# Optimization experiments

Hardware: AMD Instinct MI355X
Metric: run time of the kernel (lower is better)

The kernel has to match this reference:

```python
import jax, jax.numpy as jnp
import numpy as np
from jax import lax

TIME_DIM = 100   # time_feat_dim
MEM_DIM = 172    # node_feat_dim == memory_dim
TAU = 0.3        # energy_threshold
LAM = 0.01       # softshrink sparsity_threshold


def _layer_norm(x, w, b, eps=1e-5):
    m = x.mean(-1, keepdims=True)
    v = ((x - m) ** 2).mean(-1, keepdims=True)
    return (x - m) / jnp.sqrt(v + eps) * w + b


def _time_encode(t):
    # TGN time encoder: cos(t * 1/10^linspace(0,9,D)), fixed (non-trainable)
    freqs = 1.0 / (10.0 ** jnp.linspace(0.0, 9.0, TIME_DIM))
    return jnp.cos(t[..., None] * freqs)


def _softshrink(x, lam=LAM):
    return jnp.where(x > lam, x - lam, jnp.where(x < -lam, x + lam, 0.0))


def setup_inputs() -> dict:
    key = jax.random.key(0)
    ks = jax.random.split(key, 12)
    B, N, NUM_NODES = 8192, 32, 500000
    s = 0.02  # scale used by Global_Local_Filtering
    return {
        "node_ids": jnp.arange(B, dtype=jnp.int32),
        "neighbor_node_ids": jax.random.randint(ks[0], (B, N), 0, NUM_NODES, dtype=jnp.int32),
        "node_interact_times": jax.random.uniform(ks[1], (B,), dtype=jnp.float32) * 1000.0,
        "neighbor_times": jax.random.uniform(ks[2], (B, N), dtype=jnp.float32) * 1000.0,
        "node_memories": jnp.zeros((NUM_NODES, MEM_DIM), jnp.float32),
        "r1": s * jax.random.normal(ks[3], (TIME_DIM, MEM_DIM), jnp.float32),
        "i1": s * jax.random.normal(ks[4], (TIME_DIM, MEM_DIM), jnp.float32),
        "rb1": s * jax.random.normal(ks[5], (MEM_DIM,), jnp.float32),
        "ib1": s * jax.random.normal(ks[6], (MEM_DIM,), jnp.float32),
        "conv_w": 0.02 * jax.random.normal(ks[7], (MEM_DIM, MEM_DIM, 8), jnp.float32),
        "conv_b": 0.02 * jax.random.normal(ks[8], (MEM_DIM,), jnp.float32),
        "rhythm_w": 0.1 * jax.random.normal(ks[9], (272, 1, 4), jnp.float32),
        "lin_w": 0.05 * jax.random.normal(ks[10], (272, MEM_DIM), jnp.float32),
        "lin_b": 0.02 * jax.random.normal(ks[11], (MEM_DIM,), jnp.float32),
        "mb_ln_w": jnp.ones((MEM_DIM,), jnp.float32),
        "mb_ln_b": jnp.zeros((MEM_DIM,), jnp.float32),
        "ln_w": jnp.ones((MEM_DIM,), jnp.float32),
        "ln_b": jnp.zeros((MEM_DIM,), jnp.float32),
    }


def reference(node_ids, neighbor_node_ids, node_interact_times, neighbor_times,
              node_memories, r1, i1, rb1, ib1, conv_w, conv_b,
              rhythm_w, lin_w, lin_b, mb_ln_w, mb_ln_b, ln_w, ln_b):
    # ---- RhythmMemoryUpdater.update_memory ----
    messages = _time_encode(node_interact_times)                 # [B,100]
    old_mem = node_memories[node_ids]                            # [B,172] gather
    x = jnp.concatenate([messages, old_mem], axis=-1)[:, :, None]  # [B,272,1] (NCH)
    # depthwise Conv1d(272,272,k=4,pad=2,groups=272,no bias): length 1 -> 2
    x = lax.conv_general_dilated(x, rhythm_w, (1,), [(2, 2)],
                                 dimension_numbers=("NCH", "OIH", "NCH"),
                                 feature_group_count=272)        # [B,272,2]
    x = jnp.einsum("bcl,cd->bld", x, lin_w) + lin_b              # [B,2,172]
    new_mem = x.mean(axis=1)                                     # mean(dim=1) since 2 != memory_dim
    # set_memories: layer_norm then scatter; then gather + SeqFilter layernorm
    updated = node_memories.at[node_ids].set(_layer_norm(new_mem, mb_ln_w, mb_ln_b))
    gathered = lax.stop_gradient(updated[node_ids])              # memory bank is non-trainable (no_grad)
    root_node_time = _layer_norm(gathered, ln_w, ln_b)           # [B,172]

    # ---- neighbor branch: FSTS (Global_Local_Filtering + Conv1d) ----
    dt = node_interact_times[:, None] - neighbor_times           # [B,N]
    tfeat = _time_encode(dt)                                     # [B,N,100]
    tfeat = jnp.where((neighbor_node_ids == 0)[..., None], 0.0, tfeat)

    xf = jnp.fft.fft(tfeat, axis=1, norm="ortho")                # [B,N,100] complex
    energy = jnp.sum(jnp.abs(xf) ** 2, axis=-1)                  # [B,N]
    mask = (energy / (energy.mean() + 1e-6) >= TAU).astype(tfeat.dtype)
    low = xf * mask[..., None]
    o_r = jnp.einsum("bnc,cd->bnd", low.real, r1) - jnp.einsum("bnc,cd->bnd", low.imag, i1) + rb1
    o_i = jnp.einsum("bnc,cd->bnd", low.imag, r1) + jnp.einsum("bnc,cd->bnd", low.real, i1) + ib1
    y_fft = _softshrink(jax.nn.relu(o_r)) + 1j * _softshrink(jax.nn.relu(o_i))
    y = jnp.fft.ifft(y_fft, axis=1, norm="ortho").real           # [B,N,172]

    # Local_Correlation: Conv1d(172,172,k=8,pad=4) over neighbor axis, then mean over length
    yc = lax.conv_general_dilated(y.transpose(0, 2, 1), conv_w, (1,), [(4, 4)],
                                  dimension_numbers=("NCH", "OIH", "NCH"))
    yc = yc + conv_b[None, :, None]                              # [B,172,33]
    neighbor_out = yc.mean(axis=-1)                              # [B,172]

    return root_node_time + neighbor_out
```

## Files before the change

### kernel.cpp

```cpp
#include <hip/hip_runtime.h>
#include <hip/hip_bf16.h>
#include <math.h>

#define B_ 8192
#define NN 32
#define TD 100
#define MD 172
#define KD 1376
#define TAUC 0.3f
#define LAMC 0.01f

typedef __attribute__((ext_vector_type(8))) short short8;
typedef __attribute__((ext_vector_type(4))) float f32x4;

#define WS_U_OFF    256
#define U_BYTES     ((size_t)B_ * KD * 2)
#define CONVB_ELEMS (11 * 43 * 64 * 8)
#define WBIG_ELEMS  (22 * 7 * 64 * 8)
#define CS_ELEMS    (2 * 64 * 8)
#define ROOT_ELEMS  (11 * 9 * 64 * 8)
#define FRAG_SHORTS (CONVB_ELEMS + WBIG_ELEMS + CS_ELEMS + ROOT_ELEMS)
#define TBL_ELEMS   164

__device__ __forceinline__ float wred(float v) {
#pragma unroll
  for (int o = 32; o > 0; o >>= 1) v += __shfl_down(v, o, 64);
  return v;
}

__device__ __forceinline__ short bf16_bits(float f) {
  __hip_bfloat16 h = __float2bfloat16(f);
  return *(short*)&h;
}

__device__ __forceinline__ unsigned pack2(float a, float b) {
  return (unsigned)(unsigned short)bf16_bits(a) |
         ((unsigned)(unsigned short)bf16_bits(b) << 16);
}

__device__ __forceinline__ float fcos(float x) {
  float r = x * 0.15915494309189535f;
  r = r - floorf(r);
  return __builtin_amdgcn_cosf(r);
}

__global__ __launch_bounds__(256) void k_prep0(
    const float* __restrict__ conv_w, const float* __restrict__ r1,
    const float* __restrict__ i1, const float* __restrict__ rhythm_w,
    const float* __restrict__ lin_w, short* __restrict__ convB,
    short* __restrict__ Wfrag, short* __restrict__ CSfrag,
    short* __restrict__ Rfrag, float* __restrict__ tbl) {
  int idx = blockIdx.x * 256 + threadIdx.x;
  const float inv_s = 0.17677669529663687f;
  if (idx < CONVB_ELEMS) {
    int j = idx & 7;
    int l = (idx >> 3) & 63;
    int s = (idx >> 9) % 43;
    int n0 = idx / (43 * 64 * 8);
    int k = s * 32 + (l >> 4) * 8 + j;
    int col = n0 * 16 + (l & 15);
    float v = (col < MD) ? conv_w[(long)col * KD + k] : 0.f;
    convB[idx] = bf16_bits(v);
    return;
  }
  idx -= CONVB_ELEMS;
  if (idx < WBIG_ELEMS) {
    int j = idx & 7;
    int l = (idx >> 3) & 63;
    int s = (idx % 3584) >> 9;
    int n0 = idx / 3584;
    int k = s * 32 + (l >> 4) * 8 + j;
    int col = n0 * 16 + (l & 15);
    float v = 0.f;
    if (k < 200) {
      if (n0 < 11) {
        int d = col;
        if (d < MD) v = (k < 100) ? r1[k * MD + d] : -i1[(k - 100) * MD + d];
      } else {
        int d = col - 176;
        if (d >= 0 && d < MD) v = (k < 100) ? i1[k * MD + d] : r1[(k - 100) * MD + d];
      }
    }
    Wfrag[idx] = bf16_bits(v);
    return;
  }
  idx -= WBIG_ELEMS;
  if (idx < CS_ELEMS) {
    int j = idx & 7;
    int l = (idx >> 3) & 63;
    int s = idx >> 9;
    int row = l & 15;
    int kq = s * 32 + (l >> 4) * 8 + j;
    float v = 0.f;
    if (row < 8) {
      int kp = (kq < 32) ? kq : kq - 32;
      int lo = row - 4; if (lo < 0) lo = 0;
      int hi = row + 28; if (hi > 31) hi = 31;
      double cs = 0.0, ss = 0.0;
      for (int n = lo; n <= hi; ++n) {
        double ang = 0.19634954084936207740 * (double)((kp * n) & 31);
        cs += cos(ang); ss += sin(ang);
      }
      v = ((kq < 32) ? (float)cs : -(float)ss) * inv_s;
    }
    CSfrag[idx] = bf16_bits(v);
    return;
  }
  idx -= CS_ELEMS;
  if (idx < ROOT_ELEMS) {
    int n = idx / 4608;
    int rem = idx % 4608;
    int s = rem >> 9;
    int l = (rem >> 3) & 63;
    int j = rem & 7;
    int k = s * 32 + (l >> 4) * 8 + j;
    int col = n * 16 + (l & 15);
    float v = 0.f;
    if (k < 272 && col < MD) {
      float hw = 0.5f * (rhythm_w[k * 4 + 1] + rhythm_w[k * 4 + 2]);
      v = hw * lin_w[k * MD + col];
    }
    Rfrag[idx] = bf16_bits(v);
    return;
  }
  idx -= ROOT_ELEMS;
  if (idx < TBL_ELEMS) {
    float v;
    if (idx < 100)      v = (float)exp(-9.0 * (double)idx / 99.0 * 2.302585092994045684);
    else if (idx < 132) v = (float)cos(0.19634954084936207740 * (double)(idx - 100));
    else                v = (float)sin(0.19634954084936207740 * (double)(idx - 132));
    tbl[idx] = v;
  }
}

__global__ __launch_bounds__(256) void k_mean(const int* __restrict__ nid,
                                              const float* __restrict__ t,
                                              const float* __restrict__ nt,
                                              const float* __restrict__ tbl,
                                              float* __restrict__ ws) {
  __shared__ float fr[TD];
  __shared__ float part[4];
  int tid = threadIdx.x;
  if (tid < TD) fr[tid] = tbl[tid];
  __syncthreads();
  int idx = blockIdx.x * 256 + tid;
  int b = idx >> 5;
  float s = 0.f;
  if (nid[idx] != 0) {
    float dt = t[b] - nt[idx];
    for (int c = 0; c < TD; ++c) { float v = fcos(dt * fr[c]); s = fmaf(v, v, s); }
  }
  s = wred(s);
  if ((tid & 63) == 0) part[tid >> 6] = s;
  __syncthreads();
  if (tid == 0) atomicAdd(ws, part[0] + part[1] + part[2] + part[3]);
}

__global__ __launch_bounds__(384, 8) void k_main(
    const int* __restrict__ nbr_id, const float* __restrict__ t,
    const float* __restrict__ nt, const float* __restrict__ rb1,
    const float* __restrict__ ib1, const float* __restrict__ ws0,
    const short* __restrict__ Wfrag, const short* __restrict__ CSfrag,
    const float* __restrict__ tbl, short* __restrict__ u_out) {
  __shared__ __align__(16) short sA[32 * 232];
  __shared__ __align__(16) unsigned char s_un[12800];
  __shared__ float s_fr[TD];
  __shared__ float s_c32[32], s_s32[32], s_dt[32], s_z[32];
  __shared__ float s_energy[32];

  float* tf = (float*)s_un;
  short* Y = (short*)s_un;
  const int tid = threadIdx.x;
  const int b = blockIdx.x;
  const int l = tid & 63, w = tid >> 6;
  const float inv_s = 0.17677669529663687f;

  if (tid < 32) {
    s_c32[tid] = tbl[100 + tid];
    s_s32[tid] = tbl[132 + tid];
    int gi = b * NN + tid;
    int id = nbr_id[gi];
    float d = t[b] - nt[gi];
    s_z[tid]  = (id == 0) ? 0.f : 1.f;
    s_dt[tid] = (id == 0) ? 0.f : d;
    s_energy[tid] = 0.f;
  }
  if (tid < TD) s_fr[tid] = tbl[tid];
  __syncthreads();

  for (int idx = tid; idx < NN * TD; idx += 384) {
    int n = idx / TD, c = idx - n * TD;
    tf[idx] = s_z[n] * fcos(s_dt[n] * s_fr[c]);
  }
  if (tid < 256) {
    int row = tid >> 3, q = tid & 7;
    *(uint2*)(sA + row * 232 + 200 + q * 4) = make_uint2(0u, 0u);
  }
  __syncthreads();

  for (int task = tid; task < 17 * 25; task += 384) {
    int k = task / 25, c4 = (task - k * 25) * 4;
    float ar0=0,ar1=0,ar2=0,ar3=0, ai0=0,ai1=0,ai2=0,ai3=0;
    for (int n = 0; n < NN; ++n) {
      float4 a = *(const float4*)(tf + n * TD + c4);
      int j = (k * n) & 31;
      float cw = s_c32[j], sw = s_s32[j];
      ar0 = fmaf(a.x, cw, ar0); ai0 = fmaf(a.x, -sw, ai0);
      ar1 = fmaf(a.y, cw, ar1); ai1 = fmaf(a.y, -sw, ai1);
      ar2 = fmaf(a.z, cw, ar2); ai2 = fmaf(a.z, -sw, ai2);
      ar3 = fmaf(a.w, cw, ar3); ai3 = fmaf(a.w, -sw, ai3);
    }
    ar0*=inv_s; ar1*=inv_s; ar2*=inv_s; ar3*=inv_s;
    ai0*=inv_s; ai1*=inv_s; ai2*=inv_s; ai3*=inv_s;
    float e = ar0*ar0+ar1*ar1+ar2*ar2+ar3*ar3 + ai0*ai0+ai1*ai1+ai2*ai2+ai3*ai3;
    atomicAdd(&s_energy[k], e);
    uint2 vr = make_uint2(pack2(ar0, ar1), pack2(ar2, ar3));
    uint2 vi = make_uint2(pack2(ai0, ai1), pack2(ai2, ai3));
    *(uint2*)(sA + k * 232 + c4) = vr;
    *(uint2*)(sA + k * 232 + 100 + c4) = vi;
    if (k >= 1 && k <= 15) {
      uint2 vin = make_uint2(pack2(-ai0, -ai1), pack2(-ai2, -ai3));
      *(uint2*)(sA + (32 - k) * 232 + c4) = vr;
      *(uint2*)(sA + (32 - k) * 232 + 100 + c4) = vin;
    }
  }
  __syncthreads();

  {
    float gth = TAUC * (ws0[0] * (1.0f / 262144.0f) + 1e-6f);
    for (int idx = tid; idx < 800; idx += 384) {
      int row = idx / 25, q = idx - row * 25;
      int ks = (row <= 16) ? row : 32 - row;
      if (s_energy[ks] < gth)
        *(uint4*)((char*)sA + row * 464 + q * 16) = make_uint4(0u,0u,0u,0u);
    }
  }
  __syncthreads();

  const int mside = (w >= 3) ? 1 : 0;
  const int wn = w % 3;
  short8 afrag[7];
  {
    const short* ab = sA + (mside * 16 + (l & 15)) * 232 + ((l >> 4) << 3);
#pragma unroll
    for (int s = 0; s < 7; ++s) afrag[s] = *(const short8*)(ab + s * 32);
  }
  for (int n = wn; n < 11; n += 3) {
    f32x4 acc = (f32x4)(0.f);
#pragma unroll
    for (int s = 0; s < 7; ++s) {
      short8 bb = *(const short8*)(Wfrag + (((n * 7 + s) * 64) + l) * 8);
      acc = __builtin_amdgcn_mfma_f32_16x16x32_bf16(afrag[s], bb, acc, 0, 0, 0);
    }
    int d = n * 16 + (l & 15);
    bool valid = (d < MD);
    float bias = valid ? rb1[d] : 0.f;
    float y0 = valid ? fmaxf(acc[0] + bias - LAMC, 0.f) : 0.f;
    float y1 = valid ? fmaxf(acc[1] + bias - LAMC, 0.f) : 0.f;
    float y2 = valid ? fmaxf(acc[2] + bias - LAMC, 0.f) : 0.f;
    float y3 = valid ? fmaxf(acc[3] + bias - LAMC, 0.f) : 0.f;
    *(uint2*)(Y + d * 32 + mside * 16 + ((l >> 4) << 2)) =
        make_uint2(pack2(y0, y1), pack2(y2, y3));
  }
  __syncthreads();

  f32x4 uacc[2];
  uacc[0] = (f32x4)(0.f); uacc[1] = (f32x4)(0.f);
  {
    short8 cs0 = *(const short8*)(CSfrag + (l << 3));
#pragma unroll
    for (int ti = 0; ti < 2; ++ti) {
      int nu = w + 6 * ti;
      if (nu < 11) {
        short8 bfr = *(const short8*)(Y + (nu * 16 + (l & 15)) * 32 + ((l >> 4) << 3));
        uacc[ti] = __builtin_amdgcn_mfma_f32_16x16x32_bf16(cs0, bfr, uacc[ti], 0, 0, 0);
      }
    }
  }
  __syncthreads();

  for (int n = wn; n < 11; n += 3) {
    f32x4 acc = (f32x4)(0.f);
    int nw = n + 11;
#pragma unroll
    for (int s = 0; s < 7; ++s) {
      short8 bb = *(const short8*)(Wfrag + (((nw * 7 + s) * 64) + l) * 8);
      acc = __builtin_amdgcn_mfma_f32_16x16x32_bf16(afrag[s], bb, acc, 0, 0, 0);
    }
    int d = n * 16 + (l & 15);
    bool valid = (d < MD);
    float bias = valid ? ib1[d] : 0.f;
    float y0 = valid ? fmaxf(acc[0] + bias - LAMC, 0.f) : 0.f;
    float y1 = valid ? fmaxf(acc[1] + bias - LAMC, 0.f) : 0.f;
    float y2 = valid ? fmaxf(acc[2] + bias - LAMC, 0.f) : 0.f;
    float y3 = valid ? fmaxf(acc[3] + bias - LAMC, 0.f) : 0.f;
    *(uint2*)(Y + d * 32 + mside * 16 + ((l >> 4) << 2)) =
        make_uint2(pack2(y0, y1), pack2(y2, y3));
  }
  __syncthreads();

  {
    short8 cs1 = *(const short8*)(CSfrag + ((64 + l) << 3));
#pragma unroll
    for (int ti = 0; ti < 2; ++ti) {
      int nu = w + 6 * ti;
      if (nu < 11) {
        short8 bfr = *(const short8*)(Y + (nu * 16 + (l & 15)) * 32 + ((l >> 4) << 3));
        uacc[ti] = __builtin_amdgcn_mfma_f32_16x16x32_bf16(cs1, bfr, uacc[ti], 0, 0, 0);
        int q = l >> 4;
        int d = nu * 16 + (l & 15);
        if (q < 2 && d < MD) {
          uint2 pv = make_uint2(pack2(uacc[ti][0], uacc[ti][1]),
                                pack2(uacc[ti][2], uacc[ti][3]));
          *(uint2*)(u_out + (long)b * KD + d * 8 + q * 4) = pv;
        }
      }
    }
  }
}

__global__ __launch_bounds__(512) void k_tail(
    const int* __restrict__ node_ids, const float* __restrict__ t,
    const float* __restrict__ node_mem, const short* __restrict__ u,
    const short* __restrict__ convB, const float* __restrict__ conv_b,
    const short* __restrict__ Rfrag, const float* __restrict__ lin_b,
    const float* __restrict__ mb_w, const float* __restrict__ mb_b,
    const float* __restrict__ ln_w, const float* __restrict__ ln_b,
    const float* __restrict__ tbl, float* __restrict__ out) {
  __shared__ __align__(16) short aR[16 * 296];
  __shared__ __align__(16) float Ct[16 * 176];
  const int tid = threadIdx.x;
  const int l = tid & 63, w = tid >> 6;
  const int b0 = blockIdx.x * 16;

  for (int idx = tid; idx < 16 * 296; idx += 512) {
    int r = idx / 296, c = idx - r * 296;
    float v = 0.f;
    if (c < TD) v = fcos(t[b0 + r] * tbl[c]);
    else if (c < 272) v = node_mem[(long)node_ids[b0 + r] * MD + (c - TD)];
    aR[idx] = bf16_bits(v);
  }
  __syncthreads();

  const int cstart = (w < 5) ? w * 2 : 10;
  const int ccnt = (w < 5) ? 2 : ((w == 5) ? 1 : 0);
  f32x4 cacc[2];
  cacc[0] = (f32x4)(0.f); cacc[1] = (f32x4)(0.f);
  if (ccnt) {
    const short* ap = u + (long)(b0 + (l & 15)) * KD + ((l >> 4) << 3);
    for (int s = 0; s < 43; ++s) {
      short8 a = *(const short8*)(ap + s * 32);
#pragma unroll
      for (int tt = 0; tt < 2; ++tt) {
        if (tt < ccnt) {
          long n0 = cstart + tt;
          short8 bb = *(const short8*)(convB + ((n0 * 43 + s) * 64 + l) * 8);
          cacc[tt] = __builtin_amdgcn_mfma_f32_16x16x32_bf16(a, bb, cacc[tt], 0, 0, 0);
        }
      }
    }
  }

  const int rstart = (w == 5) ? 0 : ((w == 6) ? 3 : 7);
  const int rcnt = (w == 5) ? 3 : ((w >= 6) ? 4 : 0);
  if (rcnt) {
    f32x4 racc[4];
#pragma unroll
    for (int tt = 0; tt < 4; ++tt) racc[tt] = (f32x4)(0.f);
    const short* arp = aR + (l & 15) * 296 + ((l >> 4) << 3);
    for (int s = 0; s < 9; ++s) {
      short8 a = *(const short8*)(arp + s * 32);
#pragma unroll
      for (int tt = 0; tt < 4; ++tt) {
        if (tt < rcnt) {
          int n = rstart + tt;
          short8 bb = *(const short8*)(Rfrag + (((n * 9 + s) * 64) + l) * 8);
          racc[tt] = __builtin_amdgcn_mfma_f32_16x16x32_bf16(a, bb, racc[tt], 0, 0, 0);
        }
      }
    }
#pragma unroll
    for (int tt = 0; tt < 4; ++tt) {
      if (tt < rcnt) {
        int n = (rstart + tt) * 16 + (l & 15);
        if (n < MD) {
#pragma unroll
          for (int r = 0; r < 4; ++r)
            Ct[((l >> 4) * 4 + r) * 176 + n] = racc[tt][r];
        }
      }
    }
  }
  __syncthreads();

  if (tid < 256) {
    int r = tid >> 4, g = tid & 15;
    float v[11];
    float sm = 0.f, sq = 0.f;
#pragma unroll
    for (int j = 0; j < 11; ++j) {
      int c = g + 16 * j;
      float x = (c < MD) ? (Ct[r * 176 + c] + lin_b[c]) : 0.f;
      v[j] = x; sm += x; sq += x * x;
    }
#pragma unroll
    for (int m = 1; m < 16; m <<= 1) { sm += __shfl_xor(sm, m, 64); sq += __shfl_xor(sq, m, 64); }
    float mean = sm / 172.f;
    float rstd = rsqrtf(sq / 172.f - mean * mean + 1e-5f);
    float sm2 = 0.f, sq2 = 0.f;
#pragma unroll
    for (int j = 0; j < 11; ++j) {
      int c = g + 16 * j;
      if (c < MD) {
        float h = (v[j] - mean) * rstd * mb_w[c] + mb_b[c];
        v[j] = h; sm2 += h; sq2 += h * h;
      }
    }
#pragma unroll
    for (int m = 1; m < 16; m <<= 1) { sm2 += __shfl_xor(sm2, m, 64); sq2 += __shfl_xor(sq2, m, 64); }
    float mean2 = sm2 / 172.f;
    float rstd2 = rsqrtf(sq2 / 172.f - mean2 * mean2 + 1e-5f);
#pragma unroll
    for (int j = 0; j < 11; ++j) {
      int c = g + 16 * j;
      if (c < MD) Ct[r * 176 + c] = (v[j] - mean2) * rstd2 * ln_w[c] + ln_b[c];
    }
  }
  __syncthreads();

#pragma unroll
  for (int tt = 0; tt < 2; ++tt) {
    if (tt < ccnt) {
      int n = (cstart + tt) * 16 + (l & 15);
      if (n < MD) {
        float cb = conv_b[n];
#pragma unroll
        for (int r = 0; r < 4; ++r) {
          int mr = (l >> 4) * 4 + r;
          out[(long)(b0 + mr) * MD + n] =
              Ct[mr * 176 + n] + cacc[tt][r] * (1.0f / 33.0f) + cb;
        }
      }
    }
  }
}

extern "C" void kernel_launch(void* const* d_in, const int* in_sizes, int n_in,
                              void* d_out, int out_size, void* d_ws, size_t ws_size,
                              hipStream_t stream) {
  const int* node_ids = (const int*)d_in[0];
  const int* nbr_id   = (const int*)d_in[1];
  const float* t  = (const float*)d_in[2];
  const float* nt = (const float*)d_in[3];
  const float* node_mem = (const float*)d_in[4];
  const float* r1 = (const float*)d_in[5];
  const float* i1 = (const float*)d_in[6];
  const float* rb1 = (const float*)d_in[7];
  const float* ib1 = (const float*)d_in[8];
  const float* conv_w = (const float*)d_in[9];
  const float* conv_b = (const float*)d_in[10];
  const float* rhythm_w = (const float*)d_in[11];
  const float* lin_w = (const float*)d_in[12];
  const float* lin_b = (const float*)d_in[13];
  const float* mb_w = (const float*)d_in[14];
  const float* mb_b = (const float*)d_in[15];
  const float* ln_w = (const float*)d_in[16];
  const float* ln_b = (const float*)d_in[17];
  float* out = (float*)d_out;
  float* wsf = (float*)d_ws;

  char* base = (char*)d_ws;
  short* u      = (short*)(base + WS_U_OFF);
  short* convB  = (short*)(base + WS_U_OFF + U_BYTES);
  short* Wfrag  = convB + CONVB_ELEMS;
  short* CSfrag = Wfrag + WBIG_ELEMS;
  short* Rfrag  = CSfrag + CS_ELEMS;
  float* tbl    = (float*)(Rfrag + ROOT_ELEMS);

  hipMemsetAsync(d_ws, 0, 16, stream);
  k_prep0<<<(FRAG_SHORTS + TBL_ELEMS + 255) / 256, 256, 0, stream>>>(
      conv_w, r1, i1, rhythm_w, lin_w, convB, Wfrag, CSfrag, Rfrag, tbl);
  k_mean<<<1024, 256, 0, stream>>>(nbr_id, t, nt, tbl, wsf);
  k_main<<<B_, 384, 0, stream>>>(nbr_id, t, nt, rb1, ib1, wsf, Wfrag, CSfrag, tbl, u);
  k_tail<<<512, 512, 0, stream>>>(node_ids, t, node_mem, u, convB, conv_b,
                                  Rfrag, lin_b, mb_w, mb_b, ln_w, ln_b, tbl, out);
}
```

Measured before the change: 615.4 us.

## Split main kernel into DFT and filter kernels, drop separate energy-mean pass

Removes the k_mean kernel by having the new DFT kernel compute per-frequency energies and atomically accumulate the global energy sum. The DFT kernel writes the spectrum straight to global memory in MFMA fragment layout, and a separate filter kernel then applies the energy mask and runs the complex GEMM and inverse DFT. Each wave in the filter kernel handles one batch row with register-resident A fragments, and shares B loads across the real and imaginary outputs. The cost is a large global intermediate (about 117 MB of bf16) that is written and then read back, in exchange for dropping the redundant cosine recomputation in k_mean and improving MFMA occupancy.

```diff
diff --git a/kernel.cpp b/kernel.cpp
--- a/kernel.cpp
+++ b/kernel.cpp
@@ -21,6 +21,7 @@
 #define ROOT_ELEMS  (11 * 9 * 64 * 8)
 #define FRAG_SHORTS (CONVB_ELEMS + WBIG_ELEMS + CS_ELEMS + ROOT_ELEMS)
 #define TBL_ELEMS   164
+#define AFRAG_SHORTS_PER_B 7168
 
 __device__ __forceinline__ float wred(float v) {
 #pragma unroll
@@ -133,47 +134,23 @@
   }
 }
 
-__global__ __launch_bounds__(256) void k_mean(const int* __restrict__ nid,
-                                              const float* __restrict__ t,
-                                              const float* __restrict__ nt,
-                                              const float* __restrict__ tbl,
-                                              float* __restrict__ ws) {
-  __shared__ float fr[TD];
-  __shared__ float part[4];
-  int tid = threadIdx.x;
-  if (tid < TD) fr[tid] = tbl[tid];
-  __syncthreads();
-  int idx = blockIdx.x * 256 + tid;
-  int b = idx >> 5;
-  float s = 0.f;
-  if (nid[idx] != 0) {
-    float dt = t[b] - nt[idx];
-    for (int c = 0; c < TD; ++c) { float v = fcos(dt * fr[c]); s = fmaf(v, v, s); }
-  }
-  s = wred(s);
-  if ((tid & 63) == 0) part[tid >> 6] = s;
-  __syncthreads();
-  if (tid == 0) atomicAdd(ws, part[0] + part[1] + part[2] + part[3]);
-}
-
-__global__ __launch_bounds__(384, 8) void k_main(
+__device__ __forceinline__ void stA(short* __restrict__ ab, int k, int col, uint2 v) {
+  int mside = k >> 4, row = k & 15, s = col >> 5, q = (col >> 3) & 3, j = col & 7;
+  *(uint2*)(ab + (((mside * 7 + s) << 9) + (q << 7) + (row << 3) + j)) = v;
+}
+
+__global__ __launch_bounds__(256) void k_dft(
     const int* __restrict__ nbr_id, const float* __restrict__ t,
-    const float* __restrict__ nt, const float* __restrict__ rb1,
-    const float* __restrict__ ib1, const float* __restrict__ ws0,
-    const short* __restrict__ Wfrag, const short* __restrict__ CSfrag,
-    const float* __restrict__ tbl, short* __restrict__ u_out) {
-  __shared__ __align__(16) short sA[32 * 232];
-  __shared__ __align__(16) unsigned char s_un[12800];
+    const float* __restrict__ nt, const float* __restrict__ tbl,
+    short* __restrict__ Afrag, float* __restrict__ e_arr,
+    float* __restrict__ ws_total) {
+  __shared__ __align__(16) float tf[NN * TD];
   __shared__ float s_fr[TD];
-  __shared__ float s_c32[32], s_s32[32], s_dt[32], s_z[32];
-  __shared__ float s_energy[32];
-
-  float* tf = (float*)s_un;
-  short* Y = (short*)s_un;
+  __shared__ float s_c32[32], s_s32[32], s_dt[32], s_z[32], s_energy[32];
   const int tid = threadIdx.x;
   const int b = blockIdx.x;
-  const int l = tid & 63, w = tid >> 6;
   const float inv_s = 0.17677669529663687f;
+  short* ab = Afrag + (long)b * AFRAG_SHORTS_PER_B;
 
   if (tid < 32) {
     s_c32[tid] = tbl[100 + tid];
@@ -188,17 +165,18 @@
   if (tid < TD) s_fr[tid] = tbl[tid];
   __syncthreads();
 
-  for (int idx = tid; idx < NN * TD; idx += 384) {
+  for (int idx = tid; idx < NN * TD; idx += 256) {
     int n = idx / TD, c = idx - n * TD;
     tf[idx] = s_z[n] * fcos(s_dt[n] * s_fr[c]);
   }
-  if (tid < 256) {
-    int row = tid >> 3, q = tid & 7;
-    *(uint2*)(sA + row * 232 + 200 + q * 4) = make_uint2(0u, 0u);
-  }
-  __syncthreads();
-
-  for (int task = tid; task < 17 * 25; task += 384) {
+  if (tid < 96) {
+    int mside = tid / 48, q = 1 + (tid / 16) % 3, row = tid & 15;
+    *(uint4*)(ab + ((mside * 7 + 6) << 9) + (q << 7) + (row << 3)) =
+        make_uint4(0u, 0u, 0u, 0u);
+  }
+  __syncthreads();
+
+  for (int task = tid; task < 17 * 25; task += 256) {
     int k = task / 25, c4 = (task - k * 25) * 4;
     float ar0=0,ar1=0,ar2=0,ar3=0, ai0=0,ai1=0,ai2=0,ai3=0;
     for (int n = 0; n < NN; ++n) {
@@ -216,105 +194,96 @@
     atomicAdd(&s_energy[k], e);
     uint2 vr = make_uint2(pack2(ar0, ar1), pack2(ar2, ar3));
     uint2 vi = make_uint2(pack2(ai0, ai1), pack2(ai2, ai3));
-    *(uint2*)(sA + k * 232 + c4) = vr;
-    *(uint2*)(sA + k * 232 + 100 + c4) = vi;
+    stA(ab, k, c4, vr);
+    stA(ab, k, 100 + c4, vi);
     if (k >= 1 && k <= 15) {
       uint2 vin = make_uint2(pack2(-ai0, -ai1), pack2(-ai2, -ai3));
-      *(uint2*)(sA + (32 - k) * 232 + c4) = vr;
-      *(uint2*)(sA + (32 - k) * 232 + 100 + c4) = vin;
-    }
-  }
-  __syncthreads();
-
-  {
-    float gth = TAUC * (ws0[0] * (1.0f / 262144.0f) + 1e-6f);
-    for (int idx = tid; idx < 800; idx += 384) {
-      int row = idx / 25, q = idx - row * 25;
-      int ks = (row <= 16) ? row : 32 - row;
-      if (s_energy[ks] < gth)
-        *(uint4*)((char*)sA + row * 464 + q * 16) = make_uint4(0u,0u,0u,0u);
-    }
-  }
-  __syncthreads();
-
-  const int mside = (w >= 3) ? 1 : 0;
-  const int wn = w % 3;
-  short8 afrag[7];
-  {
-    const short* ab = sA + (mside * 16 + (l & 15)) * 232 + ((l >> 4) << 3);
-#pragma unroll
-    for (int s = 0; s < 7; ++s) afrag[s] = *(const short8*)(ab + s * 32);
-  }
-  for (int n = wn; n < 11; n += 3) {
-    f32x4 acc = (f32x4)(0.f);
+      stA(ab, 32 - k, c4, vr);
+      stA(ab, 32 - k, 100 + c4, vin);
+    }
+  }
+  __syncthreads();
+
+  if (tid < 64) {
+    float e = 0.f;
+    if (tid < 32) {
+      int ks = (tid <= 16) ? tid : 32 - tid;
+      e = s_energy[ks];
+      e_arr[b * 32 + tid] = e;
+    }
+    float s = wred(e);
+    if (tid == 0) atomicAdd(ws_total, s);
+  }
+}
+
+__global__ __launch_bounds__(256, 3) void k_filt(
+    const short* __restrict__ Afrag, const short* __restrict__ Wfrag,
+    const short* __restrict__ CSfrag, const float* __restrict__ e_arr,
+    const float* __restrict__ ws0, const float* __restrict__ rb1,
+    const float* __restrict__ ib1, short* __restrict__ u_out) {
+  __shared__ __align__(16) short scr[4][16 * 72];
+  const int tid = threadIdx.x, l = tid & 63, w = tid >> 6;
+  const long b = (long)blockIdx.x * 4 + w;
+  short* S = scr[w];
+  const int c = l & 15, q = l >> 4;
+
+  const float gth = TAUC * (ws0[0] * (1.0f / 262144.0f) + 1e-6f);
+  short8 cs0 = *(const short8*)(CSfrag + l * 8);
+  short8 cs1 = *(const short8*)(CSfrag + (64 + l) * 8);
+
+  const float e0 = e_arr[b * 32 + c];
+  const float e1 = e_arr[b * 32 + 16 + c];
+  const bool m0 = (e0 >= gth), m1 = (e1 >= gth);
+  const short* ab = Afrag + b * AFRAG_SHORTS_PER_B + l * 8;
+  short8 A0[7], A1[7];
+#pragma unroll
+  for (int s = 0; s < 7; ++s) {
+    short8 a = *(const short8*)(ab + (s << 9));
+    short8 bsh = *(const short8*)(ab + 3584 + (s << 9));
+    A0[s] = m0 ? a : (short8)0;
+    A1[s] = m1 ? bsh : (short8)0;
+  }
+
+#pragma unroll 1
+  for (int n = 0; n < 11; ++n) {
+    f32x4 a00 = (f32x4)(0.f), a10 = (f32x4)(0.f);
+    f32x4 a01 = (f32x4)(0.f), a11 = (f32x4)(0.f);
 #pragma unroll
     for (int s = 0; s < 7; ++s) {
-      short8 bb = *(const short8*)(Wfrag + (((n * 7 + s) * 64) + l) * 8);
-      acc = __builtin_amdgcn_mfma_f32_16x16x32_bf16(afrag[s], bb, acc, 0, 0, 0);
-    }
-    int d = n * 16 + (l & 15);
-    bool valid = (d < MD);
-    float bias = valid ? rb1[d] : 0.f;
-    float y0 = valid ? fmaxf(acc[0] + bias - LAMC, 0.f) : 0.f;
-    float y1 = valid ? fmaxf(acc[1] + bias - LAMC, 0.f) : 0.f;
-    float y2 = valid ? fmaxf(acc[2] + bias - LAMC, 0.f) : 0.f;
-    float y3 = valid ? fmaxf(acc[3] + bias - LAMC, 0.f) : 0.f;
-    *(uint2*)(Y + d * 32 + mside * 16 + ((l >> 4) << 2)) =
-        make_uint2(pack2(y0, y1), pack2(y2, y3));
-  }
-  __syncthreads();
-
-  f32x4 uacc[2];
-  uacc[0] = (f32x4)(0.f); uacc[1] = (f32x4)(0.f);
-  {
-    short8 cs0 = *(const short8*)(CSfrag + (l << 3));
-#pragma unroll
-    for (int ti = 0; ti < 2; ++ti) {
-      int nu = w + 6 * ti;
-      if (nu < 11) {
-        short8 bfr = *(const short8*)(Y + (nu * 16 + (l & 15)) * 32 + ((l >> 4) << 3));
-        uacc[ti] = __builtin_amdgcn_mfma_f32_16x16x32_bf16(cs0, bfr, uacc[ti], 0, 0, 0);
-      }
-    }
-  }
-  __syncthreads();
-
-  for (int n = wn; n < 11; n += 3) {
-    f32x4 acc = (f32x4)(0.f);
-    int nw = n + 11;
-#pragma unroll
-    for (int s = 0; s < 7; ++s) {
-      short8 bb = *(const short8*)(Wfrag + (((nw * 7 + s) * 64) + l) * 8);
-      acc = __builtin_amdgcn_mfma_f32_16x16x32_bf16(afrag[s], bb, acc, 0, 0, 0);
-    }
-    int d = n * 16 + (l & 15);
-    bool valid = (d < MD);
-    float bias = valid ? ib1[d] : 0.f;
-    float y0 = valid ? fmaxf(acc[0] + bias - LAMC, 0.f) : 0.f;
-    float y1 = valid ? fmaxf(acc[1] + bias - LAMC, 0.f) : 0.f;
-    float y2 = valid ? fmaxf(acc[2] + bias - LAMC, 0.f) : 0.f;
-    float y3 = valid ? fmaxf(acc[3] + bias - LAMC, 0.f) : 0.f;
-    *(uint2*)(Y + d * 32 + mside * 16 + ((l >> 4) << 2)) =
-        make_uint2(pack2(y0, y1), pack2(y2, y3));
-  }
-  __syncthreads();
-
-  {
-    short8 cs1 = *(const short8*)(CSfrag + ((64 + l) << 3));
-#pragma unroll
-    for (int ti = 0; ti < 2; ++ti) {
-      int nu = w + 6 * ti;
-      if (nu < 11) {
-        short8 bfr = *(const short8*)(Y + (nu * 16 + (l & 15)) * 32 + ((l >> 4) << 3));
-        uacc[ti] = __builtin_amdgcn_mfma_f32_16x16x32_bf16(cs1, bfr, uacc[ti], 0, 0, 0);
-        int q = l >> 4;
-        int d = nu * 16 + (l & 15);
-        if (q < 2 && d < MD) {
-          uint2 pv = make_uint2(pack2(uacc[ti][0], uacc[ti][1]),
-                                pack2(uacc[ti][2], uacc[ti][3]));
-          *(uint2*)(u_out + (long)b * KD + d * 8 + q * 4) = pv;
-        }
-      }
+      short8 b0 = *(const short8*)(Wfrag + (((n * 7 + s) << 6) + l) * 8);
+      short8 b1 = *(const short8*)(Wfrag + ((((n + 11) * 7 + s) << 6) + l) * 8);
+      a00 = __builtin_amdgcn_mfma_f32_16x16x32_bf16(A0[s], b0, a00, 0, 0, 0);
+      a10 = __builtin_amdgcn_mfma_f32_16x16x32_bf16(A1[s], b0, a10, 0, 0, 0);
+      a01 = __builtin_amdgcn_mfma_f32_16x16x32_bf16(A0[s], b1, a01, 0, 0, 0);
+      a11 = __builtin_amdgcn_mfma_f32_16x16x32_bf16(A1[s], b1, a11, 0, 0, 0);
+    }
+    const int d = n * 16 + c;
+    const bool valid = (d < MD);
+    const float br = valid ? rb1[d] : 0.f;
+    const float bi = valid ? ib1[d] : 0.f;
+    f32x4 y00, y10, y01, y11;
+#pragma unroll
+    for (int r = 0; r < 4; ++r) {
+      y00[r] = valid ? fmaxf(a00[r] + br - LAMC, 0.f) : 0.f;
+      y10[r] = valid ? fmaxf(a10[r] + br - LAMC, 0.f) : 0.f;
+      y01[r] = valid ? fmaxf(a01[r] + bi - LAMC, 0.f) : 0.f;
+      y11[r] = valid ? fmaxf(a11[r] + bi - LAMC, 0.f) : 0.f;
+    }
+    asm volatile("s_waitcnt lgkmcnt(0)" ::: "memory");
+    short* Sc = S + c * 72 + q * 4;
+    *(uint2*)(Sc)      = make_uint2(pack2(y00[0], y00[1]), pack2(y00[2], y00[3]));
+    *(uint2*)(Sc + 16) = make_uint2(pack2(y10[0], y10[1]), pack2(y10[2], y10[3]));
+    *(uint2*)(Sc + 32) = make_uint2(pack2(y01[0], y01[1]), pack2(y01[2], y01[3]));
+    *(uint2*)(Sc + 48) = make_uint2(pack2(y11[0], y11[1]), pack2(y11[2], y11[3]));
+    asm volatile("s_waitcnt lgkmcnt(0)" ::: "memory");
+    short8 Br = *(const short8*)(S + c * 72 + q * 8);
+    short8 Bi = *(const short8*)(S + c * 72 + 32 + q * 8);
+    f32x4 u = (f32x4)(0.f);
+    u = __builtin_amdgcn_mfma_f32_16x16x32_bf16(cs0, Br, u, 0, 0, 0);
+    u = __builtin_amdgcn_mfma_f32_16x16x32_bf16(cs1, Bi, u, 0, 0, 0);
+    if (q < 2 && valid) {
+      uint2 pv = make_uint2(pack2(u[0], u[1]), pack2(u[2], u[3]));
+      *(uint2*)(u_out + b * KD + d * 8 + q * 4) = pv;
     }
   }
 }
@@ -476,12 +445,17 @@
   short* CSfrag = Wfrag + WBIG_ELEMS;
   short* Rfrag  = CSfrag + CS_ELEMS;
   float* tbl    = (float*)(Rfrag + ROOT_ELEMS);
+  size_t off = (size_t)((char*)(tbl + TBL_ELEMS) - base);
+  off = (off + 255) & ~(size_t)255;
+  short* Afrag = (short*)(base + off);
+  float* e_arr = (float*)(base + off + (size_t)B_ * AFRAG_SHORTS_PER_B * 2);
 
   hipMemsetAsync(d_ws, 0, 16, stream);
   k_prep0<<<(FRAG_SHORTS + TBL_ELEMS + 255) / 256, 256, 0, stream>>>(
       conv_w, r1, i1, rhythm_w, lin_w, convB, Wfrag, CSfrag, Rfrag, tbl);
-  k_mean<<<1024, 256, 0, stream>>>(nbr_id, t, nt, tbl, wsf);
-  k_main<<<B_, 384, 0, stream>>>(nbr_id, t, nt, rb1, ib1, wsf, Wfrag, CSfrag, tbl, u);
+  k_dft<<<B_, 256, 0, stream>>>(nbr_id, t, nt, tbl, Afrag, e_arr, wsf);
+  k_filt<<<B_ / 4, 256, 0, stream>>>(Afrag, Wfrag, CSfrag, e_arr, wsf,
+                                     rb1, ib1, u);
   k_tail<<<512, 512, 0, stream>>>(node_ids, t, node_mem, u, convB, conv_b,
                                   Rfrag, lin_b, mb_w, mb_b, ln_w, ln_b, tbl, out);
 }
```

Measured after the change: 636.4 us. 1.03x slower.

## Rebalance MFMA work across waves in main and tail kernels

Applied to the files above, without the earlier changes.

In k_main, each wave now loads both 16-row halves of the spectral A-matrix and computes two output column tiles, so each Wfrag B-fragment load is reused for two MFMAs. Previously the six waves were split by row half and column stride. The occupancy hint drops from 8 to 4 blocks to leave room for the larger register set. In k_tail the block grows to 1024 threads: 11 waves each take one conv output tile and 5 waves share the root projection tiles, which evens out per-wave MFMA chains. Lower occupancy in k_main may reduce latency hiding for its global loads.

```diff
diff --git a/kernel.cpp b/kernel.cpp
--- a/kernel.cpp
+++ b/kernel.cpp
@@ -156,7 +156,7 @@
   if (tid == 0) atomicAdd(ws, part[0] + part[1] + part[2] + part[3]);
 }
 
-__global__ __launch_bounds__(384, 8) void k_main(
+__global__ __launch_bounds__(384, 4) void k_main(
     const int* __restrict__ nbr_id, const float* __restrict__ t,
     const float* __restrict__ nt, const float* __restrict__ rb1,
     const float* __restrict__ ib1, const float* __restrict__ ws0,
@@ -173,6 +173,7 @@
   const int tid = threadIdx.x;
   const int b = blockIdx.x;
   const int l = tid & 63, w = tid >> 6;
+  const int c = l & 15, q = l >> 4;
   const float inv_s = 0.17677669529663687f;
 
   if (tid < 32) {
@@ -189,12 +190,12 @@
   __syncthreads();
 
   for (int idx = tid; idx < NN * TD; idx += 384) {
-    int n = idx / TD, c = idx - n * TD;
-    tf[idx] = s_z[n] * fcos(s_dt[n] * s_fr[c]);
+    int n = idx / TD, cc = idx - n * TD;
+    tf[idx] = s_z[n] * fcos(s_dt[n] * s_fr[cc]);
   }
   if (tid < 256) {
-    int row = tid >> 3, q = tid & 7;
-    *(uint2*)(sA + row * 232 + 200 + q * 4) = make_uint2(0u, 0u);
+    int row = tid >> 3, qq = tid & 7;
+    *(uint2*)(sA + row * 232 + 200 + qq * 4) = make_uint2(0u, 0u);
   }
   __syncthreads();
 
@@ -229,38 +230,48 @@
   {
     float gth = TAUC * (ws0[0] * (1.0f / 262144.0f) + 1e-6f);
     for (int idx = tid; idx < 800; idx += 384) {
-      int row = idx / 25, q = idx - row * 25;
+      int row = idx / 25, qq = idx - row * 25;
       int ks = (row <= 16) ? row : 32 - row;
       if (s_energy[ks] < gth)
-        *(uint4*)((char*)sA + row * 464 + q * 16) = make_uint4(0u,0u,0u,0u);
-    }
-  }
-  __syncthreads();
-
-  const int mside = (w >= 3) ? 1 : 0;
-  const int wn = w % 3;
-  short8 afrag[7];
+        *(uint4*)((char*)sA + row * 464 + qq * 16) = make_uint4(0u,0u,0u,0u);
+    }
+  }
+  __syncthreads();
+
+  short8 A0[7], A1[7];
   {
-    const short* ab = sA + (mside * 16 + (l & 15)) * 232 + ((l >> 4) << 3);
-#pragma unroll
-    for (int s = 0; s < 7; ++s) afrag[s] = *(const short8*)(ab + s * 32);
-  }
-  for (int n = wn; n < 11; n += 3) {
-    f32x4 acc = (f32x4)(0.f);
+    const short* a0 = sA + c * 232 + (q << 3);
+    const short* a1 = sA + (16 + c) * 232 + (q << 3);
 #pragma unroll
     for (int s = 0; s < 7; ++s) {
-      short8 bb = *(const short8*)(Wfrag + (((n * 7 + s) * 64) + l) * 8);
-      acc = __builtin_amdgcn_mfma_f32_16x16x32_bf16(afrag[s], bb, acc, 0, 0, 0);
-    }
-    int d = n * 16 + (l & 15);
-    bool valid = (d < MD);
-    float bias = valid ? rb1[d] : 0.f;
-    float y0 = valid ? fmaxf(acc[0] + bias - LAMC, 0.f) : 0.f;
-    float y1 = valid ? fmaxf(acc[1] + bias - LAMC, 0.f) : 0.f;
-    float y2 = valid ? fmaxf(acc[2] + bias - LAMC, 0.f) : 0.f;
-    float y3 = valid ? fmaxf(acc[3] + bias - LAMC, 0.f) : 0.f;
-    *(uint2*)(Y + d * 32 + mside * 16 + ((l >> 4) << 2)) =
-        make_uint2(pack2(y0, y1), pack2(y2, y3));
+      A0[s] = *(const short8*)(a0 + s * 32);
+      A1[s] = *(const short8*)(a1 + s * 32);
+    }
+  }
+
+#pragma unroll
+  for (int rep = 0; rep < 2; ++rep) {
+    int n = w + 6 * rep;
+    if (n < 11) {
+      f32x4 acc0 = (f32x4)(0.f), acc1 = (f32x4)(0.f);
+#pragma unroll
+      for (int s = 0; s < 7; ++s) {
+        short8 bb = *(const short8*)(Wfrag + (((n * 7 + s) << 6) + l) * 8);
+        acc0 = __builtin_amdgcn_mfma_f32_16x16x32_bf16(A0[s], bb, acc0, 0, 0, 0);
+        acc1 = __builtin_amdgcn_mfma_f32_16x16x32_bf16(A1[s], bb, acc1, 0, 0, 0);
+      }
+      int d = n * 16 + c;
+      bool valid = (d < MD);
+      float bias = valid ? rb1[d] : 0.f;
+      f32x4 y0, y1;
+#pragma unroll
+      for (int r = 0; r < 4; ++r) {
+        y0[r] = valid ? fmaxf(acc0[r] + bias - LAMC, 0.f) : 0.f;
+        y1[r] = valid ? fmaxf(acc1[r] + bias - LAMC, 0.f) : 0.f;
+      }
+      *(uint2*)(Y + d * 32 + (q << 2))      = make_uint2(pack2(y0[0], y0[1]), pack2(y0[2], y0[3]));
+      *(uint2*)(Y + d * 32 + 16 + (q << 2)) = make_uint2(pack2(y1[0], y1[1]), pack2(y1[2], y1[3]));
+    }
   }
   __syncthreads();
 
@@ -272,30 +283,37 @@
     for (int ti = 0; ti < 2; ++ti) {
       int nu = w + 6 * ti;
       if (nu < 11) {
-        short8 bfr = *(const short8*)(Y + (nu * 16 + (l & 15)) * 32 + ((l >> 4) << 3));
+        short8 bfr = *(const short8*)(Y + (nu * 16 + c) * 32 + (q << 3));
         uacc[ti] = __builtin_amdgcn_mfma_f32_16x16x32_bf16(cs0, bfr, uacc[ti], 0, 0, 0);
       }
     }
   }
   __syncthreads();
 
-  for (int n = wn; n < 11; n += 3) {
-    f32x4 acc = (f32x4)(0.f);
-    int nw = n + 11;
-#pragma unroll
-    for (int s = 0; s < 7; ++s) {
-      short8 bb = *(const short8*)(Wfrag + (((nw * 7 + s) * 64) + l) * 8);
-      acc = __builtin_amdgcn_mfma_f32_16x16x32_bf16(afrag[s], bb, acc, 0, 0, 0);
-    }
-    int d = n * 16 + (l & 15);
-    bool valid = (d < MD);
-    float bias = valid ? ib1[d] : 0.f;
-    float y0 = valid ? fmaxf(acc[0] + bias - LAMC, 0.f) : 0.f;
-    float y1 = valid ? fmaxf(acc[1] + bias - LAMC, 0.f) : 0.f;
-    float y2 = valid ? fmaxf(acc[2] + bias - LAMC, 0.f) : 0.f;
-    float y3 = valid ? fmaxf(acc[3] + bias - LAMC, 0.f) : 0.f;
-    *(uint2*)(Y + d * 32 + mside * 16 + ((l >> 4) << 2)) =
-        make_uint2(pack2(y0, y1), pack2(y2, y3));
+#pragma unroll
+  for (int rep = 0; rep < 2; ++rep) {
+    int n = w + 6 * rep;
+    if (n < 11) {
+      int nw = n + 11;
+      f32x4 acc0 = (f32x4)(0.f), acc1 = (f32x4)(0.f);
+#pragma unroll
+      for (int s = 0; s < 7; ++s) {
+        short8 bb = *(const short8*)(Wfrag + (((nw * 7 + s) << 6) + l) * 8);
+        acc0 = __builtin_amdgcn_mfma_f32_16x16x32_bf16(A0[s], bb, acc0, 0, 0, 0);
+        acc1 = __builtin_amdgcn_mfma_f32_16x16x32_bf16(A1[s], bb, acc1, 0, 0, 0);
+      }
+      int d = n * 16 + c;
+      bool valid = (d < MD);
+      float bias = valid ? ib1[d] : 0.f;
+      f32x4 y0, y1;
+#pragma unroll
+      for (int r = 0; r < 4; ++r) {
+        y0[r] = valid ? fmaxf(acc0[r] + bias - LAMC, 0.f) : 0.f;
+        y1[r] = valid ? fmaxf(acc1[r] + bias - LAMC, 0.f) : 0.f;
+      }
+      *(uint2*)(Y + d * 32 + (q << 2))      = make_uint2(pack2(y0[0], y0[1]), pack2(y0[2], y0[3]));
+      *(uint2*)(Y + d * 32 + 16 + (q << 2)) = make_uint2(pack2(y1[0], y1[1]), pack2(y1[2], y1[3]));
+    }
   }
   __syncthreads();
 
@@ -305,10 +323,9 @@
     for (int ti = 0; ti < 2; ++ti) {
       int nu = w + 6 * ti;
       if (nu < 11) {
-        short8 bfr = *(const short8*)(Y + (nu * 16 + (l & 15)) * 32 + ((l >> 4) << 3));
+        short8 bfr = *(const short8*)(Y + (nu * 16 + c) * 32 + (q << 3));
         uacc[ti] = __builtin_amdgcn_mfma_f32_16x16x32_bf16(cs1, bfr, uacc[ti], 0, 0, 0);
-        int q = l >> 4;
-        int d = nu * 16 + (l & 15);
+        int d = nu * 16 + c;
         if (q < 2 && d < MD) {
           uint2 pv = make_uint2(pack2(uacc[ti][0], uacc[ti][1]),
                                 pack2(uacc[ti][2], uacc[ti][3]));
@@ -319,7 +336,7 @@
   }
 }
 
-__global__ __launch_bounds__(512) void k_tail(
+__global__ __launch_bounds__(1024) void k_tail(
     const int* __restrict__ node_ids, const float* __restrict__ t,
     const float* __restrict__ node_mem, const short* __restrict__ u,
     const short* __restrict__ convB, const float* __restrict__ conv_b,
@@ -331,47 +348,39 @@
   __shared__ __align__(16) float Ct[16 * 176];
   const int tid = threadIdx.x;
   const int l = tid & 63, w = tid >> 6;
+  const int c = l & 15, q = l >> 4;
   const int b0 = blockIdx.x * 16;
 
-  for (int idx = tid; idx < 16 * 296; idx += 512) {
-    int r = idx / 296, c = idx - r * 296;
+  for (int idx = tid; idx < 16 * 296; idx += 1024) {
+    int r = idx / 296, cc = idx - r * 296;
     float v = 0.f;
-    if (c < TD) v = fcos(t[b0 + r] * tbl[c]);
-    else if (c < 272) v = node_mem[(long)node_ids[b0 + r] * MD + (c - TD)];
+    if (cc < TD) v = fcos(t[b0 + r] * tbl[cc]);
+    else if (cc < 272) v = node_mem[(long)node_ids[b0 + r] * MD + (cc - TD)];
     aR[idx] = bf16_bits(v);
   }
   __syncthreads();
 
-  const int cstart = (w < 5) ? w * 2 : 10;
-  const int ccnt = (w < 5) ? 2 : ((w == 5) ? 1 : 0);
-  f32x4 cacc[2];
-  cacc[0] = (f32x4)(0.f); cacc[1] = (f32x4)(0.f);
-  if (ccnt) {
-    const short* ap = u + (long)(b0 + (l & 15)) * KD + ((l >> 4) << 3);
+  f32x4 cacc = (f32x4)(0.f);
+  if (w < 11) {
+    const short* ap = u + (long)(b0 + c) * KD + (q << 3);
+    const short* bp = convB + (((long)w * 43) * 64 + l) * 8;
+#pragma unroll 4
     for (int s = 0; s < 43; ++s) {
       short8 a = *(const short8*)(ap + s * 32);
-#pragma unroll
-      for (int tt = 0; tt < 2; ++tt) {
-        if (tt < ccnt) {
-          long n0 = cstart + tt;
-          short8 bb = *(const short8*)(convB + ((n0 * 43 + s) * 64 + l) * 8);
-          cacc[tt] = __builtin_amdgcn_mfma_f32_16x16x32_bf16(a, bb, cacc[tt], 0, 0, 0);
-        }
-      }
-    }
-  }
-
-  const int rstart = (w == 5) ? 0 : ((w == 6) ? 3 : 7);
-  const int rcnt = (w == 5) ? 3 : ((w >= 6) ? 4 : 0);
-  if (rcnt) {
-    f32x4 racc[4];
-#pragma unroll
-    for (int tt = 0; tt < 4; ++tt) racc[tt] = (f32x4)(0.f);
-    const short* arp = aR + (l & 15) * 296 + ((l >> 4) << 3);
+      short8 bb = *(const short8*)(bp + (s << 9));
+      cacc = __builtin_amdgcn_mfma_f32_16x16x32_bf16(a, bb, cacc, 0, 0, 0);
+    }
+  } else {
+    const int rstart = (w - 11) * 2;
+    const int rcnt = (w == 15) ? 3 : 2;
+    f32x4 racc[3];
+#pragma unroll
+    for (int tt = 0; tt < 3; ++tt) racc[tt] = (f32x4)(0.f);
+    const short* arp = aR + c * 296 + (q << 3);
     for (int s = 0; s < 9; ++s) {
       short8 a = *(const short8*)(arp + s * 32);
 #pragma unroll
-      for (int tt = 0; tt < 4; ++tt) {
+      for (int tt = 0; tt < 3; ++tt) {
         if (tt < rcnt) {
           int n = rstart + tt;
           short8 bb = *(const short8*)(Rfrag + (((n * 9 + s) * 64) + l) * 8);
@@ -380,14 +389,12 @@
       }
     }
 #pragma unroll
-    for (int tt = 0; tt < 4; ++tt) {
+    for (int tt = 0; tt < 3; ++tt) {
       if (tt < rcnt) {
-        int n = (rstart + tt) * 16 + (l & 15);
-        if (n < MD) {
-#pragma unroll
-          for (int r = 0; r < 4; ++r)
-            Ct[((l >> 4) * 4 + r) * 176 + n] = racc[tt][r];
-        }
+        int n = (rstart + tt) * 16 + c;
+#pragma unroll
+        for (int r = 0; r < 4; ++r)
+          Ct[(q * 4 + r) * 176 + n] = racc[tt][r];
       }
     }
   }
@@ -399,8 +406,8 @@
     float sm = 0.f, sq = 0.f;
 #pragma unroll
     for (int j = 0; j < 11; ++j) {
-      int c = g + 16 * j;
-      float x = (c < MD) ? (Ct[r * 176 + c] + lin_b[c]) : 0.f;
+      int cc = g + 16 * j;
+      float x = (cc < MD) ? (Ct[r * 176 + cc] + lin_b[cc]) : 0.f;
       v[j] = x; sm += x; sq += x * x;
     }
 #pragma unroll
@@ -410,9 +417,9 @@
     float sm2 = 0.f, sq2 = 0.f;
 #pragma unroll
     for (int j = 0; j < 11; ++j) {
-      int c = g + 16 * j;
-      if (c < MD) {
-        float h = (v[j] - mean) * rstd * mb_w[c] + mb_b[c];
+      int cc = g + 16 * j;
+      if (cc < MD) {
+        float h = (v[j] - mean) * rstd * mb_w[cc] + mb_b[cc];
         v[j] = h; sm2 += h; sq2 += h * h;
       }
     }
@@ -422,24 +429,21 @@
     float rstd2 = rsqrtf(sq2 / 172.f - mean2 * mean2 + 1e-5f);
 #pragma unroll
     for (int j = 0; j < 11; ++j) {
-      int c = g + 16 * j;
-      if (c < MD) Ct[r * 176 + c] = (v[j] - mean2) * rstd2 * ln_w[c] + ln_b[c];
-    }
-  }
-  __syncthreads();
-
-#pragma unroll
-  for (int tt = 0; tt < 2; ++tt) {
-    if (tt < ccnt) {
-      int n = (cstart + tt) * 16 + (l & 15);
-      if (n < MD) {
-        float cb = conv_b[n];
-#pragma unroll
-        for (int r = 0; r < 4; ++r) {
-          int mr = (l >> 4) * 4 + r;
-          out[(long)(b0 + mr) * MD + n] =
-              Ct[mr * 176 + n] + cacc[tt][r] * (1.0f / 33.0f) + cb;
-        }
+      int cc = g + 16 * j;
+      if (cc < MD) Ct[r * 176 + cc] = (v[j] - mean2) * rstd2 * ln_w[cc] + ln_b[cc];
+    }
+  }
+  __syncthreads();
+
+  if (w < 11) {
+    int n = w * 16 + c;
+    if (n < MD) {
+      float cb = conv_b[n];
+#pragma unroll
+      for (int r = 0; r < 4; ++r) {
+        int mr = q * 4 + r;
+        out[(long)(b0 + mr) * MD + n] =
+            Ct[mr * 176 + n] + cacc[r] * (1.0f / 33.0f) + cb;
       }
     }
   }
@@ -482,6 +486,6 @@
       conv_w, r1, i1, rhythm_w, lin_w, convB, Wfrag, CSfrag, Rfrag, tbl);
   k_mean<<<1024, 256, 0, stream>>>(nbr_id, t, nt, tbl, wsf);
   k_main<<<B_, 384, 0, stream>>>(nbr_id, t, nt, rb1, ib1, wsf, Wfrag, CSfrag, tbl, u);
-  k_tail<<<512, 512, 0, stream>>>(node_ids, t, node_mem, u, convB, conv_b,
-                                  Rfrag, lin_b, mb_w, mb_b, ln_w, ln_b, tbl, out);
-}
+  k_tail<<<512, 1024, 0, stream>>>(node_ids, t, node_mem, u, convB, conv_b,
+                                   Rfrag, lin_b, mb_w, mb_b, ln_w, ln_b, tbl, out);
+}
```

Result: slower. 634.3 us (+3.1%).
